# Kernel optimization log

Measured on AMD Instinct MI355X. Metric: run time of the kernel, lower is better.

The kernel has to match this reference:

```python
import jax, jax.numpy as jnp
import numpy as np
import math

B, T, D = 4, 4096, 256


def setup_inputs() -> dict:
    key = jax.random.key(0)
    ks = jax.random.split(key, 12)
    stdv = 1.0 / math.sqrt(D)
    u = lambda k, shape, s: jax.random.uniform(k, shape, jnp.float32, -s, s)
    return {
        "query": jax.random.normal(ks[0], (B, T, D), jnp.float32),
        "value": jax.random.normal(ks[1], (B, T, D), jnp.float32),
        # gate vectors, init uniform(-1/sqrt(D), 1/sqrt(D)) per reset_parameters
        "q_vec": u(ks[2], (D,), stdv),
        "k_vec": u(ks[3], (D,), stdv),
        "v_vec": u(ks[4], (D,), stdv),
        # nn.Linear params (torch default init: uniform(-1/sqrt(fan_in), ...))
        "Wq": u(ks[5], (D, D), stdv), "bq": u(ks[6], (D,), stdv),
        "Ws": u(ks[7], (D, D), stdv), "bs": u(ks[8], (D,), stdv),
        "Wt": u(ks[9], (D, D), stdv), "bt": u(ks[10], (D,), stdv),
    }


def reference(query, value, q_vec, k_vec, v_vec, Wq, bq, Ws, bs, Wt, bt):
    d = query.shape[-1]
    # q = Linear(query) * sigmoid(query_vector)
    q = (jnp.einsum('btd,ed->bte', query, Wq) + bq) * jax.nn.sigmoid(q_vec)
    # k = value * sigmoid(key_vector)
    k = value * jax.nn.sigmoid(k_vec)
    # v gate: infer=False branch -> GLU-style gate of sigmoid(value_vector)
    vv = jax.nn.sigmoid(v_vec)
    v_gate = jax.nn.sigmoid(Ws @ vv + bs) * jnp.tanh(Wt @ vv + bt)
    v = value * v_gate
    # scores [B, T, T]
    w = jnp.einsum('bqd,bkd->bqk', q, k) / jnp.sqrt(jnp.float32(d))
    # causal: multiply by tril mask then replace exact zeros with -inf
    # (faithful to the original's weight[weight==0]=-inf quirk)
    Tn = w.shape[-1]
    tril = jnp.tril(jnp.ones((Tn, Tn), w.dtype))
    w = w * tril
    w = jnp.where(w == 0.0, -jnp.inf, w)
    attn = jax.nn.softmax(w, axis=-1)
    return jnp.einsum('bqk,bkd->bqd', attn, v)
```

## Files before the change

### kernel.cpp

```cpp
#include <hip/hip_runtime.h>
#include <math.h>

#define D 256
#define T 4096
#define KT (17408/2)
#define VT (20480/2)
#define PSTR ((size_t)4*T*D)

typedef __attribute__((ext_vector_type(8))) short bf16x8;
typedef __attribute__((ext_vector_type(4))) float f32x4;
typedef __attribute__((ext_vector_type(8))) unsigned short u16x8;
typedef __attribute__((ext_vector_type(4))) unsigned int u32x4;

#define QSCALE 0.0901684850f

__device__ __forceinline__ unsigned short f2bf(float x){
  unsigned int u = __float_as_uint(x);
  unsigned int r = (u + 0x7FFFu + ((u >> 16) & 1u)) >> 16;
  return (unsigned short)r;
}
__device__ __forceinline__ float bf2f(unsigned short h){
  return __uint_as_float(((unsigned int)h) << 16);
}
__device__ __forceinline__ unsigned int cvtpk(float lo, float hi){
  unsigned int w;
  asm("v_cvt_pk_bf16_f32 %0, %1, %2" : "=v"(w) : "v"(lo), "v"(hi));
  return w;
}

__device__ __forceinline__ void gl_lds16(const void* g, void* l){
  __builtin_amdgcn_global_load_lds((const __attribute__((address_space(1))) unsigned int*)g,
                                   (__attribute__((address_space(3))) unsigned int*)l, 16, 0, 0);
}

__global__ __launch_bounds__(256) void prep_kernel(
    const float* __restrict__ q_vec, const float* __restrict__ k_vec,
    const float* __restrict__ v_vec, const float* __restrict__ Ws,
    const float* __restrict__ bs, const float* __restrict__ Wt,
    const float* __restrict__ bt, const float* __restrict__ Wq,
    float* __restrict__ gates, unsigned short* __restrict__ wq_g){
  int t = threadIdx.x;
  if(blockIdx.x == 0){
    __shared__ float vv[D];
    vv[t]         = 1.f/(1.f + __expf(-v_vec[t]));
    gates[t]      = 1.f/(1.f + __expf(-q_vec[t]));
    gates[D + t]  = 1.f/(1.f + __expf(-k_vec[t]));
    __syncthreads();
    const f32x4* wsr = (const f32x4*)(Ws + (size_t)t*D);
    const f32x4* wtr = (const f32x4*)(Wt + (size_t)t*D);
    const f32x4* vvv = (const f32x4*)vv;
    f32x4 a0 = {0,0,0,0}, a1 = {0,0,0,0}, c0 = {0,0,0,0}, c1 = {0,0,0,0};
    for(int i=0;i<64;i+=2){
      f32x4 v0 = vvv[i], v1 = vvv[i+1];
      a0 += wsr[i]*v0; a1 += wsr[i+1]*v1;
      c0 += wtr[i]*v0; c1 += wtr[i+1]*v1;
    }
    f32x4 as = a0 + a1, cs = c0 + c1;
    float s1 = bs[t] + as[0]+as[1]+as[2]+as[3];
    float s2 = bt[t] + cs[0]+cs[1]+cs[2]+cs[3];
    gates[2*D + t] = (1.f/(1.f + __expf(-s1))) * tanhf(s2);
  } else {
    int kc = blockIdx.x - 1;
    const float* src = Wq + (size_t)t*D + kc*32;
    unsigned short* dst = wq_g + (size_t)kc*10240 + t*40;
    #pragma unroll
    for(int u=0;u<4;u++){
      bf16x8 pk;
      #pragma unroll
      for(int x=0;x<8;x++) pk[x] = (short)f2bf(src[u*8+x]);
      *(bf16x8*)&dst[u*8] = pk;
    }
  }
}

__global__ __launch_bounds__(256) void mid_kernel(
    const float* __restrict__ query, const unsigned short* __restrict__ wq_g,
    const float* __restrict__ bq, const float* __restrict__ gates,
    unsigned short* __restrict__ q_g,
    const float* __restrict__ value,
    unsigned short* __restrict__ k_g, unsigned short* __restrict__ vt_g){
  __shared__ __align__(16) unsigned short smem[2][10240];
  int tid = threadIdx.x;
  if(blockIdx.x < 256){
    int w = tid >> 6; int l = tid & 63;
    int lr = l & 15, lc = l >> 4;
    int r0 = blockIdx.x * 64;
    f32x4 acc[16];
    #pragma unroll
    for(int n=0;n<16;n++) acc[n] = (f32x4){0.f,0.f,0.f,0.f};
    const float* qrow = query + (size_t)(r0 + w*16 + lr)*D;
    #pragma unroll
    for(int i=0;i<5;i++){ int c = i*256 + tid; gl_lds16(wq_g + c*8, (char*)smem[0] + c*16); }
    __syncthreads();
    int cur = 0;
    for(int kc=0; kc<8; kc++){
      if(kc < 7){
        #pragma unroll
        for(int i=0;i<5;i++){ int c = i*256 + tid;
          gl_lds16(wq_g + (size_t)(kc+1)*10240 + c*8, (char*)smem[cur^1] + c*16); }
      }
      bf16x8 af;
      {
        const float* s = qrow + kc*32 + lc*8;
        #pragma unroll
        for(int x=0;x<8;x++) af[x] = (short)f2bf(s[x]);
      }
      #pragma unroll
      for(int n=0;n<16;n++){
        bf16x8 bfrag = *(const bf16x8*)&smem[cur][(n*16 + lr)*40 + lc*8];
        acc[n] = __builtin_amdgcn_mfma_f32_16x16x32_bf16(af, bfrag, acc[n], 0, 0, 0);
      }
      __syncthreads();
      cur ^= 1;
    }
    #pragma unroll
    for(int n=0;n<16;n++){
      int col = n*16 + lr;
      float bb = bq[col], gg = gates[col] * QSCALE;
      #pragma unroll
      for(int r=0;r<4;r++){
        int row = r0 + w*16 + lc*4 + r;
        q_g[(size_t)row*D + col] = f2bf((acc[n][r] + bb) * gg);
      }
    }
  } else {
    int bid2 = blockIdx.x - 256;
    int b = bid2 >> 7, jt = bid2 & 127;
    const float* vbase = value + ((size_t)b*T + jt*32)*D;
    const float* gk = gates + D;
    const float* vg = gates + 2*D;
    unsigned short* kt = k_g  + (size_t)bid2 * KT;
    unsigned short* vt = vt_g + (size_t)bid2 * VT;
    #pragma unroll
    for(int i=0;i<4;i++){
      int g = i*256 + tid; int j = g >> 5, c = g & 31;
      const float* src = vbase + j*D + c*8;
      bf16x8 pk;
      #pragma unroll
      for(int x=0;x<8;x++) pk[x] = (short)f2bf(src[x] * gk[c*8+x]);
      *(bf16x8*)&kt[j*264 + c*8] = pk;
    }
    float* lds = (float*)smem;
    for(int c=0;c<4;c++){
      __syncthreads();
      {
        int row = tid >> 3, cg = tid & 7;
        const float* src = vbase + (size_t)row*D + c*64 + cg*8;
        f32x4 v0 = *(const f32x4*)src;
        f32x4 v1 = *(const f32x4*)(src + 4);
        *(f32x4*)&lds[row*68 + cg*8]     = v0;
        *(f32x4*)&lds[row*68 + cg*8 + 4] = v1;
      }
      __syncthreads();
      {
        int d0l = tid >> 2, u = tid & 3;
        int d0 = c*64 + d0l;
        float gd = vg[d0];
        bf16x8 pk;
        #pragma unroll
        for(int x=0;x<8;x++){
          int p = u*8 + x;
          int ksrc = ((p>>3)<<2) + (p&3) + (((p>>2)&1)<<4);
          pk[x] = (short)f2bf(lds[ksrc*68 + d0l] * gd);
        }
        *(bf16x8*)&vt[d0*40 + u*8] = pk;
      }
    }
  }
}

__global__ __launch_bounds__(256, 2) void flash_kernel(
    const unsigned short* __restrict__ q_g,
    const unsigned short* __restrict__ k_g,
    const unsigned short* __restrict__ vt_g,
    unsigned short* __restrict__ parts,
    float* __restrict__ ml, int logS){
  __shared__ __align__(16) unsigned short kbuf[2][KT];
  __shared__ __align__(16) unsigned short vbuf[2][VT];
  int tid = threadIdx.x; int w = tid >> 6, l = tid & 63;
  int lr = l & 15, lc = l >> 4;
  int S = 1 << logS;
  int bid = blockIdx.x;
  int x = bid & 7; int b = x >> 1; int p = x & 1;
  int item = bid >> 3;
  int half = S >> 1;
  int rblk = 31 - (item / half);
  int s = p*half + (item % half);
  int r0 = rblk * 128;
  int wrow0 = r0 + w*32;
  int nt = 4*rblk + 4;
  int jt0 = (s*nt) >> logS, jt1 = ((s+1)*nt) >> logS;
  int grA = wrow0 + lr;
  int grB = wrow0 + 16 + lr;
  int diagA = (wrow0 + 15) >> 5;
  int diagB = (wrow0 + 31) >> 5;

  bf16x8 qfA[8], qfB[8];
  {
    const unsigned short* qa = q_g + ((size_t)b*T + grA)*D + lc*8;
    const unsigned short* qb = q_g + ((size_t)b*T + grB)*D + lc*8;
    #pragma unroll
    for(int kc=0;kc<8;kc++){
      qfA[kc] = *(const bf16x8*)(qa + kc*32);
      qfB[kc] = *(const bf16x8*)(qb + kc*32);
    }
  }
  f32x4 oA[16], oB[16];
  #pragma unroll
  for(int n=0;n<16;n++){ oA[n] = (f32x4){0.f,0.f,0.f,0.f}; oB[n] = (f32x4){0.f,0.f,0.f,0.f}; }
  float mA = -INFINITY, lsA = 0.f, mB = -INFINITY, lsB = 0.f;

  const unsigned short* ktb = k_g  + (size_t)b*128*KT;
  const unsigned short* vtb = vt_g + (size_t)b*128*VT;

  if(jt1 > jt0){
    const unsigned short* ks = ktb + (size_t)jt0*KT;
    const unsigned short* vs = vtb + (size_t)jt0*VT;
    for(int c=w; c<37; c+=4){
      if(c < 17) gl_lds16(ks + c*512 + l*8, (char*)kbuf[jt0&1] + c*1024);
      else       gl_lds16(vs + (c-17)*512 + l*8, (char*)vbuf[jt0&1] + (c-17)*1024);
    }
  }

  for(int jt=jt0; jt<jt1; jt++){
    int cur = jt & 1;
    asm volatile("s_waitcnt vmcnt(0)" ::: "memory");
    __builtin_amdgcn_s_barrier();
    __builtin_amdgcn_sched_barrier(0);
    if(jt+1 < jt1){
      const unsigned short* ks = ktb + (size_t)(jt+1)*KT;
      const unsigned short* vs = vtb + (size_t)(jt+1)*VT;
      for(int c=w; c<37; c+=4){
        if(c < 17) gl_lds16(ks + c*512 + l*8, (char*)kbuf[cur^1] + c*1024);
        else       gl_lds16(vs + (c-17)*512 + l*8, (char*)vbuf[cur^1] + (c-17)*1024);
      }
    }
    int j0 = jt*32;
    bool actA = (j0 <= wrow0 + 15);
    bool actB = (j0 <= wrow0 + 31);
    if(actB){
      f32x4 sA0={0,0,0,0}, sA1={0,0,0,0}, sB0={0,0,0,0}, sB1={0,0,0,0};
      if(actA){
        #pragma unroll
        for(int kc=0;kc<8;kc++){
          bf16x8 k0 = *(const bf16x8*)&kbuf[cur][lr*264        + (kc*4 + lc)*8];
          bf16x8 k1 = *(const bf16x8*)&kbuf[cur][(16 + lr)*264 + (kc*4 + lc)*8];
          sA0 = __builtin_amdgcn_mfma_f32_16x16x32_bf16(k0, qfA[kc], sA0, 0,0,0);
          sA1 = __builtin_amdgcn_mfma_f32_16x16x32_bf16(k1, qfA[kc], sA1, 0,0,0);
          sB0 = __builtin_amdgcn_mfma_f32_16x16x32_bf16(k0, qfB[kc], sB0, 0,0,0);
          sB1 = __builtin_amdgcn_mfma_f32_16x16x32_bf16(k1, qfB[kc], sB1, 0,0,0);
        }
      } else {
        #pragma unroll
        for(int kc=0;kc<8;kc++){
          bf16x8 k0 = *(const bf16x8*)&kbuf[cur][lr*264        + (kc*4 + lc)*8];
          bf16x8 k1 = *(const bf16x8*)&kbuf[cur][(16 + lr)*264 + (kc*4 + lc)*8];
          sB0 = __builtin_amdgcn_mfma_f32_16x16x32_bf16(k0, qfB[kc], sB0, 0,0,0);
          sB1 = __builtin_amdgcn_mfma_f32_16x16x32_bf16(k1, qfB[kc], sB1, 0,0,0);
        }
      }
      bf16x8 paA, paB;
      if(actA){
        float sv0[4], sv1[4];
        if(jt == diagA){
          #pragma unroll
          for(int r=0;r<4;r++){
            float x0 = sA0[r]; int gj0 = j0 + lc*4 + r;
            float x1 = sA1[r]; int gj1 = gj0 + 16;
            sv0[r] = (gj0 > grA || x0 == 0.0f) ? -INFINITY : x0;
            sv1[r] = (gj1 > grA || x1 == 0.0f) ? -INFINITY : x1;
          }
        } else {
          #pragma unroll
          for(int r=0;r<4;r++){
            sv0[r] = (sA0[r] == 0.0f) ? -INFINITY : sA0[r];
            sv1[r] = (sA1[r] == 0.0f) ? -INFINITY : sA1[r];
          }
        }
        float pmax = fmaxf(fmaxf(fmaxf(sv0[0],sv0[1]),fmaxf(sv0[2],sv0[3])),
                           fmaxf(fmaxf(sv1[0],sv1[1]),fmaxf(sv1[2],sv1[3])));
        pmax = fmaxf(pmax, __shfl_xor(pmax, 16));
        pmax = fmaxf(pmax, __shfl_xor(pmax, 32));
        bool mv = (pmax > mA + 11.5f);
        float mn = mv ? pmax : mA;
        float alpha = mv ? exp2f(mA - mn) : 1.0f;
        float p0[4], p1[4];
        #pragma unroll
        for(int r=0;r<4;r++){
          p0[r] = exp2f(sv0[r] - mn);
          p1[r] = exp2f(sv1[r] - mn);
        }
        if(__builtin_amdgcn_ballot_w64(mv)){
          float a0 = __shfl(alpha, lc*4 + 0);
          float a1 = __shfl(alpha, lc*4 + 1);
          float a2 = __shfl(alpha, lc*4 + 2);
          float a3 = __shfl(alpha, lc*4 + 3);
          #pragma unroll
          for(int n=0;n<16;n++){
            oA[n][0] *= a0; oA[n][1] *= a1; oA[n][2] *= a2; oA[n][3] *= a3;
          }
        }
        float ps = ((p0[0]+p0[1])+(p0[2]+p0[3])) + ((p1[0]+p1[1])+(p1[2]+p1[3]));
        lsA = lsA*alpha + ps;
        mA = mn;
        union { unsigned int u[4]; bf16x8 h; } pu;
        pu.u[0] = cvtpk(p0[0], p0[1]); pu.u[1] = cvtpk(p0[2], p0[3]);
        pu.u[2] = cvtpk(p1[0], p1[1]); pu.u[3] = cvtpk(p1[2], p1[3]);
        paA = pu.h;
      }
      {
        float sv0[4], sv1[4];
        if(jt == diagB){
          #pragma unroll
          for(int r=0;r<4;r++){
            float x0 = sB0[r]; int gj0 = j0 + lc*4 + r;
            float x1 = sB1[r]; int gj1 = gj0 + 16;
            sv0[r] = (gj0 > grB || x0 == 0.0f) ? -INFINITY : x0;
            sv1[r] = (gj1 > grB || x1 == 0.0f) ? -INFINITY : x1;
          }
        } else {
          #pragma unroll
          for(int r=0;r<4;r++){
            sv0[r] = (sB0[r] == 0.0f) ? -INFINITY : sB0[r];
            sv1[r] = (sB1[r] == 0.0f) ? -INFINITY : sB1[r];
          }
        }
        float pmax = fmaxf(fmaxf(fmaxf(sv0[0],sv0[1]),fmaxf(sv0[2],sv0[3])),
                           fmaxf(fmaxf(sv1[0],sv1[1]),fmaxf(sv1[2],sv1[3])));
        pmax = fmaxf(pmax, __shfl_xor(pmax, 16));
        pmax = fmaxf(pmax, __shfl_xor(pmax, 32));
        bool mv = (pmax > mB + 11.5f);
        float mn = mv ? pmax : mB;
        float alpha = mv ? exp2f(mB - mn) : 1.0f;
        float p0[4], p1[4];
        #pragma unroll
        for(int r=0;r<4;r++){
          p0[r] = exp2f(sv0[r] - mn);
          p1[r] = exp2f(sv1[r] - mn);
        }
        if(__builtin_amdgcn_ballot_w64(mv)){
          float a0 = __shfl(alpha, lc*4 + 0);
          float a1 = __shfl(alpha, lc*4 + 1);
          float a2 = __shfl(alpha, lc*4 + 2);
          float a3 = __shfl(alpha, lc*4 + 3);
          #pragma unroll
          for(int n=0;n<16;n++){
            oB[n][0] *= a0; oB[n][1] *= a1; oB[n][2] *= a2; oB[n][3] *= a3;
          }
        }
        float ps = ((p0[0]+p0[1])+(p0[2]+p0[3])) + ((p1[0]+p1[1])+(p1[2]+p1[3]));
        lsB = lsB*alpha + ps;
        mB = mn;
        union { unsigned int u[4]; bf16x8 h; } pu;
        pu.u[0] = cvtpk(p0[0], p0[1]); pu.u[1] = cvtpk(p0[2], p0[3]);
        pu.u[2] = cvtpk(p1[0], p1[1]); pu.u[3] = cvtpk(p1[2], p1[3]);
        paB = pu.h;
      }
      if(actA){
        #pragma unroll
        for(int n=0;n<16;n++){
          bf16x8 vf = *(const bf16x8*)&vbuf[cur][(n*16 + lr)*40 + lc*8];
          oA[n] = __builtin_amdgcn_mfma_f32_16x16x32_bf16(paA, vf, oA[n], 0,0,0);
          oB[n] = __builtin_amdgcn_mfma_f32_16x16x32_bf16(paB, vf, oB[n], 0,0,0);
        }
      } else {
        #pragma unroll
        for(int n=0;n<16;n++){
          bf16x8 vf = *(const bf16x8*)&vbuf[cur][(n*16 + lr)*40 + lc*8];
          oB[n] = __builtin_amdgcn_mfma_f32_16x16x32_bf16(paB, vf, oB[n], 0,0,0);
        }
      }
    }
  }

  unsigned short* obase = parts + (size_t)s*PSTR + ((size_t)b*T + wrow0)*D;
  #pragma unroll
  for(int r=0;r<4;r++){
    int row = lc*4 + r;
    unsigned int wa[8], wb[8];
    #pragma unroll
    for(int k=0;k<8;k++){
      wa[k] = cvtpk(oA[2*k][r], oA[2*k+1][r]);
      wb[k] = cvtpk(oB[2*k][r], oB[2*k+1][r]);
    }
    *(u32x4*)&obase[(size_t)row*D + lr*16]          = (u32x4){wa[0],wa[1],wa[2],wa[3]};
    *(u32x4*)&obase[(size_t)row*D + lr*16 + 8]      = (u32x4){wa[4],wa[5],wa[6],wa[7]};
    *(u32x4*)&obase[(size_t)(row+16)*D + lr*16]     = (u32x4){wb[0],wb[1],wb[2],wb[3]};
    *(u32x4*)&obase[(size_t)(row+16)*D + lr*16 + 8] = (u32x4){wb[4],wb[5],wb[6],wb[7]};
  }
  lsA += __shfl_xor(lsA, 16); lsA += __shfl_xor(lsA, 32);
  lsB += __shfl_xor(lsB, 16); lsB += __shfl_xor(lsB, 32);
  if(l < 16){
    float* mlbA = ml + ((size_t)s*4*T + (size_t)b*T + wrow0 + lr)*2;
    mlbA[0] = mA; mlbA[1] = lsA;
    float* mlbB = ml + ((size_t)s*4*T + (size_t)b*T + wrow0 + 16 + lr)*2;
    mlbB[0] = mB; mlbB[1] = lsB;
  }
}

__global__ __launch_bounds__(256) void combine_kernel(
    const unsigned short* __restrict__ parts, const float* __restrict__ ml,
    float* __restrict__ out, int S){
  int t = blockIdx.x*256 + threadIdx.x;
  int row = t >> 4;
  int lr  = t & 15;
  float msv[8], lsv[8];
  float mm = -INFINITY;
  #pragma unroll
  for(int s=0;s<8;s++){
    if(s >= S) break;
    msv[s] = ml[((size_t)s*4*T + row)*2];
    lsv[s] = ml[((size_t)s*4*T + row)*2 + 1];
    mm = fmaxf(mm, msv[s]);
  }
  float denom = 0.f;
  float acc[16];
  #pragma unroll
  for(int n=0;n<16;n++) acc[n] = 0.f;
  #pragma unroll
  for(int s=0;s<8;s++){
    if(s >= S) break;
    float as = exp2f(msv[s] - mm);
    if(as != 0.0f){
      denom += as*lsv[s];
      const unsigned short* src = parts + (size_t)s*PSTR + (size_t)row*D + lr*16;
      u16x8 v0 = *(const u16x8*)src;
      u16x8 v1 = *(const u16x8*)(src + 8);
      #pragma unroll
      for(int n=0;n<8;n++){ acc[n] += as*bf2f(v0[n]); acc[8+n] += as*bf2f(v1[n]); }
    }
  }
  float inv = 1.0f/denom;
  float* orow = out + (size_t)row*D;
  #pragma unroll
  for(int n=0;n<16;n++) orow[n*16 + lr] = acc[n]*inv;
}

extern "C" void kernel_launch(void* const* d_in, const int* in_sizes, int n_in,
                              void* d_out, int out_size, void* d_ws, size_t ws_size,
                              hipStream_t stream){
  (void)in_sizes; (void)n_in; (void)out_size;
  const float* query = (const float*)d_in[0];
  const float* value = (const float*)d_in[1];
  const float* q_vec = (const float*)d_in[2];
  const float* k_vec = (const float*)d_in[3];
  const float* v_vec = (const float*)d_in[4];
  const float* Wq    = (const float*)d_in[5];
  const float* bq    = (const float*)d_in[6];
  const float* Ws    = (const float*)d_in[7];
  const float* bs    = (const float*)d_in[8];
  const float* Wt    = (const float*)d_in[9];
  const float* bt    = (const float*)d_in[10];
  char* ws = (char*)d_ws;
  unsigned short* q_g  = (unsigned short*)(ws);
  unsigned short* k_g  = (unsigned short*)(ws + 8388608);
  unsigned short* vt_g = (unsigned short*)(ws + 17301504);
  unsigned short* wq_g = (unsigned short*)(ws + 27787264);
  float* gates         = (float*)(ws + 27951104);
  unsigned short* parts= (unsigned short*)(ws + 27955200);
  float* out = (float*)d_out;

  size_t base = 27955200;
  size_t mlsz = (size_t)8*4*T*2*4;
  int logS;
  if(ws_size >= base + 8*PSTR*2 + mlsz)      logS = 3;
  else if(ws_size >= base + 4*PSTR*2 + mlsz) logS = 2;
  else                                       logS = 1;
  int S = 1 << logS;
  float* ml = (float*)(ws + base + (size_t)S*PSTR*2);

  hipLaunchKernelGGL(prep_kernel, dim3(9),   dim3(256), 0, stream,
                     q_vec, k_vec, v_vec, Ws, bs, Wt, bt, Wq, gates, wq_g);
  hipLaunchKernelGGL(mid_kernel,  dim3(768), dim3(256), 0, stream,
                     query, wq_g, bq, gates, q_g, value, k_g, vt_g);
  hipLaunchKernelGGL(flash_kernel, dim3(128*S), dim3(256), 0, stream,
                     q_g, k_g, vt_g, parts, ml, logS);
  hipLaunchKernelGGL(combine_kernel, dim3((4*T*16)/256), dim3(256), 0, stream,
                     parts, ml, out, S);
}
```

Baseline: 113.6 us.

## Fuse split-KV combine into flash kernel via last-block atomic counter

Removes the separate combine kernel. Each flash block bumps a per-(batch,row-block) atomic counter, and the last split to finish merges all partial outputs for that 128-row block and writes the final result. The work-to-block mapping also changes so the split index is the fastest-varying part of the block id, with row blocks interleaved by parity. This saves one launch and lets the combine overlap with other blocks, but it adds a memset, a fence plus atomic per block, and a serial tail in which a single block does the combine.

```diff
diff --git a/kernel.cpp b/kernel.cpp
--- a/kernel.cpp
+++ b/kernel.cpp
@@ -174,18 +174,20 @@
     const unsigned short* __restrict__ k_g,
     const unsigned short* __restrict__ vt_g,
     unsigned short* __restrict__ parts,
-    float* __restrict__ ml, int logS){
+    float* __restrict__ ml, unsigned int* __restrict__ cnt,
+    float* __restrict__ out, int logS){
   __shared__ __align__(16) unsigned short kbuf[2][KT];
   __shared__ __align__(16) unsigned short vbuf[2][VT];
+  __shared__ unsigned int lastflag;
   int tid = threadIdx.x; int w = tid >> 6, l = tid & 63;
   int lr = l & 15, lc = l >> 4;
   int S = 1 << logS;
   int bid = blockIdx.x;
-  int x = bid & 7; int b = x >> 1; int p = x & 1;
+  int x = bid & 7; int b = x >> 1; int par = x & 1;
   int item = bid >> 3;
-  int half = S >> 1;
-  int rblk = 31 - (item / half);
-  int s = p*half + (item % half);
+  int rl = item >> logS;
+  int rblk = (par ? 31 : 30) - 2*rl;
+  int s = item & (S - 1);
   int r0 = rblk * 128;
   int wrow0 = r0 + w*32;
   int nt = 4*rblk + 4;
@@ -396,44 +398,52 @@
     float* mlbB = ml + ((size_t)s*4*T + (size_t)b*T + wrow0 + 16 + lr)*2;
     mlbB[0] = mB; mlbB[1] = lsB;
   }
-}
-
-__global__ __launch_bounds__(256) void combine_kernel(
-    const unsigned short* __restrict__ parts, const float* __restrict__ ml,
-    float* __restrict__ out, int S){
-  int t = blockIdx.x*256 + threadIdx.x;
-  int row = t >> 4;
-  int lr  = t & 15;
-  float msv[8], lsv[8];
-  float mm = -INFINITY;
-  #pragma unroll
-  for(int s=0;s<8;s++){
-    if(s >= S) break;
-    msv[s] = ml[((size_t)s*4*T + row)*2];
-    lsv[s] = ml[((size_t)s*4*T + row)*2 + 1];
-    mm = fmaxf(mm, msv[s]);
-  }
-  float denom = 0.f;
-  float acc[16];
-  #pragma unroll
-  for(int n=0;n<16;n++) acc[n] = 0.f;
-  #pragma unroll
-  for(int s=0;s<8;s++){
-    if(s >= S) break;
-    float as = exp2f(msv[s] - mm);
-    if(as != 0.0f){
-      denom += as*lsv[s];
-      const unsigned short* src = parts + (size_t)s*PSTR + (size_t)row*D + lr*16;
-      u16x8 v0 = *(const u16x8*)src;
-      u16x8 v1 = *(const u16x8*)(src + 8);
-      #pragma unroll
-      for(int n=0;n<8;n++){ acc[n] += as*bf2f(v0[n]); acc[8+n] += as*bf2f(v1[n]); }
-    }
-  }
-  float inv = 1.0f/denom;
-  float* orow = out + (size_t)row*D;
-  #pragma unroll
-  for(int n=0;n<16;n++) orow[n*16 + lr] = acc[n]*inv;
+
+  __syncthreads();
+  if(tid == 0){
+    __threadfence();
+    unsigned int old = __hip_atomic_fetch_add(&cnt[b*32 + rblk], 1u,
+                         __ATOMIC_ACQ_REL, __HIP_MEMORY_SCOPE_AGENT);
+    lastflag = (old == (unsigned)(S - 1)) ? 1u : 0u;
+  }
+  __syncthreads();
+  if(!lastflag) return;
+
+  for(int it=0; it<8; it++){
+    int t2 = it*256 + tid;
+    int row = b*T + r0 + (t2 >> 4);
+    int lr2 = t2 & 15;
+    float msv[8], lsv[8];
+    float mm = -INFINITY;
+    #pragma unroll
+    for(int s2=0; s2<8; s2++){
+      if(s2 >= S) break;
+      msv[s2] = ml[((size_t)s2*4*T + row)*2];
+      lsv[s2] = ml[((size_t)s2*4*T + row)*2 + 1];
+      mm = fmaxf(mm, msv[s2]);
+    }
+    float denom = 0.f;
+    float acc[16];
+    #pragma unroll
+    for(int n=0;n<16;n++) acc[n] = 0.f;
+    #pragma unroll
+    for(int s2=0; s2<8; s2++){
+      if(s2 >= S) break;
+      float as = exp2f(msv[s2] - mm);
+      if(as != 0.0f){
+        denom += as*lsv[s2];
+        const unsigned short* src = parts + (size_t)s2*PSTR + (size_t)row*D + lr2*16;
+        u16x8 v0 = *(const u16x8*)src;
+        u16x8 v1 = *(const u16x8*)(src + 8);
+        #pragma unroll
+        for(int n=0;n<8;n++){ acc[n] += as*bf2f(v0[n]); acc[8+n] += as*bf2f(v1[n]); }
+      }
+    }
+    float inv = 1.0f/denom;
+    float* orow = out + (size_t)row*D;
+    #pragma unroll
+    for(int n=0;n<16;n++) orow[n*16 + lr2] = acc[n]*inv;
+  }
 }
 
 extern "C" void kernel_launch(void* const* d_in, const int* in_sizes, int n_in,
@@ -463,18 +473,18 @@
   size_t base = 27955200;
   size_t mlsz = (size_t)8*4*T*2*4;
   int logS;
-  if(ws_size >= base + 8*PSTR*2 + mlsz)      logS = 3;
-  else if(ws_size >= base + 4*PSTR*2 + mlsz) logS = 2;
-  else                                       logS = 1;
+  if(ws_size >= base + 8*PSTR*2 + mlsz + 512)      logS = 3;
+  else if(ws_size >= base + 4*PSTR*2 + mlsz + 512) logS = 2;
+  else                                             logS = 1;
   int S = 1 << logS;
   float* ml = (float*)(ws + base + (size_t)S*PSTR*2);
-
+  unsigned int* cnt = (unsigned int*)(ws + base + (size_t)S*PSTR*2 + mlsz);
+
+  hipMemsetAsync(cnt, 0, 512, stream);
   hipLaunchKernelGGL(prep_kernel, dim3(9),   dim3(256), 0, stream,
                      q_vec, k_vec, v_vec, Ws, bs, Wt, bt, Wq, gates, wq_g);
   hipLaunchKernelGGL(mid_kernel,  dim3(768), dim3(256), 0, stream,
                      query, wq_g, bq, gates, q_g, value, k_g, vt_g);
   hipLaunchKernelGGL(flash_kernel, dim3(128*S), dim3(256), 0, stream,
-                     q_g, k_g, vt_g, parts, ml, logS);
-  hipLaunchKernelGGL(combine_kernel, dim3((4*T*16)/256), dim3(256), 0, stream,
-                     parts, ml, out, S);
-}
+                     q_g, k_g, vt_g, parts, ml, cnt, out, logS);
+}
```

Result: slower. 225.7 us (+98.7%).

## Compute QK^T scores with FP8 MFMA using FP8 Q and swizzled FP8 K

Applied to the files above, without the earlier changes.

Q and K are now stored as FP8 instead of BF16. The score product uses the 16x16x32 fp8 MFMA, and the softmax scale is applied after the matmul instead of being folded into Q. K tiles drop their padded row stride and use an XOR swizzle for LDS bank-conflict avoidance, which halves K load traffic and LDS footprint per tile. This risks accuracy loss from FP8 quantization and may change which scores compare exactly equal to zero.

```diff
diff --git a/kernel.cpp b/kernel.cpp
--- a/kernel.cpp
+++ b/kernel.cpp
@@ -3,7 +3,7 @@
 
 #define D 256
 #define T 4096
-#define KT (17408/2)
+#define KTB 8192
 #define VT (20480/2)
 #define PSTR ((size_t)4*T*D)
 
@@ -25,6 +25,11 @@
 __device__ __forceinline__ unsigned int cvtpk(float lo, float hi){
   unsigned int w;
   asm("v_cvt_pk_bf16_f32 %0, %1, %2" : "=v"(w) : "v"(lo), "v"(hi));
+  return w;
+}
+__device__ __forceinline__ unsigned int cvtpk8(float lo, float hi){
+  unsigned int w;
+  asm("v_cvt_pk_fp8_f32 %0, %1, %2" : "=v"(w) : "v"(lo), "v"(hi));
   return w;
 }
 
@@ -76,9 +81,9 @@
 __global__ __launch_bounds__(256) void mid_kernel(
     const float* __restrict__ query, const unsigned short* __restrict__ wq_g,
     const float* __restrict__ bq, const float* __restrict__ gates,
-    unsigned short* __restrict__ q_g,
+    unsigned char* __restrict__ q8,
     const float* __restrict__ value,
-    unsigned short* __restrict__ k_g, unsigned short* __restrict__ vt_g){
+    unsigned char* __restrict__ k8, unsigned short* __restrict__ vt_g){
   __shared__ __align__(16) unsigned short smem[2][10240];
   int tid = threadIdx.x;
   if(blockIdx.x < 256){
@@ -116,12 +121,18 @@
     #pragma unroll
     for(int n=0;n<16;n++){
       int col = n*16 + lr;
-      float bb = bq[col], gg = gates[col] * QSCALE;
-      #pragma unroll
-      for(int r=0;r<4;r++){
-        int row = r0 + w*16 + lc*4 + r;
-        q_g[(size_t)row*D + col] = f2bf((acc[n][r] + bb) * gg);
-      }
+      float bb = bq[col], gg = gates[col];
+      float v0 = (acc[n][0] + bb) * gg;
+      float v1 = (acc[n][1] + bb) * gg;
+      float v2 = (acc[n][2] + bb) * gg;
+      float v3 = (acc[n][3] + bb) * gg;
+      unsigned int wlo = cvtpk8(v0, v1);
+      unsigned int whi = cvtpk8(v2, v3);
+      int row0 = r0 + w*16 + lc*4;
+      q8[(size_t)(row0+0)*D + col] = (unsigned char)(wlo);
+      q8[(size_t)(row0+1)*D + col] = (unsigned char)(wlo >> 8);
+      q8[(size_t)(row0+2)*D + col] = (unsigned char)(whi);
+      q8[(size_t)(row0+3)*D + col] = (unsigned char)(whi >> 8);
     }
   } else {
     int bid2 = blockIdx.x - 256;
@@ -129,16 +140,23 @@
     const float* vbase = value + ((size_t)b*T + jt*32)*D;
     const float* gk = gates + D;
     const float* vg = gates + 2*D;
-    unsigned short* kt = k_g  + (size_t)bid2 * KT;
+    unsigned char* kt = k8 + (size_t)bid2 * KTB;
     unsigned short* vt = vt_g + (size_t)bid2 * VT;
     #pragma unroll
     for(int i=0;i<4;i++){
       int g = i*256 + tid; int j = g >> 5, c = g & 31;
       const float* src = vbase + j*D + c*8;
-      bf16x8 pk;
+      float f[8];
       #pragma unroll
-      for(int x=0;x<8;x++) pk[x] = (short)f2bf(src[x] * gk[c*8+x]);
-      *(bf16x8*)&kt[j*264 + c*8] = pk;
+      for(int x=0;x<8;x++) f[x] = src[x] * gk[c*8+x];
+      unsigned int a0 = cvtpk8(f[0], f[1]);
+      unsigned int a1 = cvtpk8(f[2], f[3]);
+      unsigned int a2 = cvtpk8(f[4], f[5]);
+      unsigned int a3 = cvtpk8(f[6], f[7]);
+      unsigned long lo = (unsigned long)((a0 & 0xffffu) | (a1 << 16));
+      unsigned long hi = (unsigned long)((a2 & 0xffffu) | (a3 << 16));
+      unsigned int off = (unsigned)(c*8) ^ (unsigned)((j & 7) << 3);
+      *(unsigned long*)&kt[(size_t)j*256 + off] = lo | (hi << 32);
     }
     float* lds = (float*)smem;
     for(int c=0;c<4;c++){
@@ -170,12 +188,12 @@
 }
 
 __global__ __launch_bounds__(256, 2) void flash_kernel(
-    const unsigned short* __restrict__ q_g,
-    const unsigned short* __restrict__ k_g,
+    const unsigned char* __restrict__ q8,
+    const unsigned char* __restrict__ k8,
     const unsigned short* __restrict__ vt_g,
     unsigned short* __restrict__ parts,
     float* __restrict__ ml, int logS){
-  __shared__ __align__(16) unsigned short kbuf[2][KT];
+  __shared__ __align__(16) unsigned char kbuf8[2][KTB];
   __shared__ __align__(16) unsigned short vbuf[2][VT];
   int tid = threadIdx.x; int w = tid >> 6, l = tid & 63;
   int lr = l & 15, lc = l >> 4;
@@ -195,14 +213,14 @@
   int diagA = (wrow0 + 15) >> 5;
   int diagB = (wrow0 + 31) >> 5;
 
-  bf16x8 qfA[8], qfB[8];
+  long qfA[8], qfB[8];
   {
-    const unsigned short* qa = q_g + ((size_t)b*T + grA)*D + lc*8;
-    const unsigned short* qb = q_g + ((size_t)b*T + grB)*D + lc*8;
+    const unsigned char* qa = q8 + ((size_t)b*T + grA)*D + lc*8;
+    const unsigned char* qb = q8 + ((size_t)b*T + grB)*D + lc*8;
     #pragma unroll
     for(int kc=0;kc<8;kc++){
-      qfA[kc] = *(const bf16x8*)(qa + kc*32);
-      qfB[kc] = *(const bf16x8*)(qb + kc*32);
+      qfA[kc] = *(const long*)(qa + kc*32);
+      qfB[kc] = *(const long*)(qb + kc*32);
     }
   }
   f32x4 oA[16], oB[16];
@@ -210,15 +228,15 @@
   for(int n=0;n<16;n++){ oA[n] = (f32x4){0.f,0.f,0.f,0.f}; oB[n] = (f32x4){0.f,0.f,0.f,0.f}; }
   float mA = -INFINITY, lsA = 0.f, mB = -INFINITY, lsB = 0.f;
 
-  const unsigned short* ktb = k_g  + (size_t)b*128*KT;
+  const unsigned char*  ktb = k8   + (size_t)b*128*KTB;
   const unsigned short* vtb = vt_g + (size_t)b*128*VT;
 
   if(jt1 > jt0){
-    const unsigned short* ks = ktb + (size_t)jt0*KT;
+    const unsigned char*  ks = ktb + (size_t)jt0*KTB;
     const unsigned short* vs = vtb + (size_t)jt0*VT;
-    for(int c=w; c<37; c+=4){
-      if(c < 17) gl_lds16(ks + c*512 + l*8, (char*)kbuf[jt0&1] + c*1024);
-      else       gl_lds16(vs + (c-17)*512 + l*8, (char*)vbuf[jt0&1] + (c-17)*1024);
+    for(int c=w; c<28; c+=4){
+      if(c < 8) gl_lds16(ks + c*1024 + l*16, (char*)kbuf8[jt0&1] + c*1024);
+      else      gl_lds16(vs + (c-8)*512 + l*8, (char*)vbuf[jt0&1] + (c-8)*1024);
     }
   }
 
@@ -228,35 +246,39 @@
     __builtin_amdgcn_s_barrier();
     __builtin_amdgcn_sched_barrier(0);
     if(jt+1 < jt1){
-      const unsigned short* ks = ktb + (size_t)(jt+1)*KT;
+      const unsigned char*  ks = ktb + (size_t)(jt+1)*KTB;
       const unsigned short* vs = vtb + (size_t)(jt+1)*VT;
-      for(int c=w; c<37; c+=4){
-        if(c < 17) gl_lds16(ks + c*512 + l*8, (char*)kbuf[cur^1] + c*1024);
-        else       gl_lds16(vs + (c-17)*512 + l*8, (char*)vbuf[cur^1] + (c-17)*1024);
+      for(int c=w; c<28; c+=4){
+        if(c < 8) gl_lds16(ks + c*1024 + l*16, (char*)kbuf8[cur^1] + c*1024);
+        else      gl_lds16(vs + (c-8)*512 + l*8, (char*)vbuf[cur^1] + (c-8)*1024);
       }
     }
     int j0 = jt*32;
     bool actA = (j0 <= wrow0 + 15);
     bool actB = (j0 <= wrow0 + 31);
     if(actB){
+      const unsigned char* kb = kbuf8[cur];
+      unsigned soff = ((unsigned)(lr & 7)) << 3;
       f32x4 sA0={0,0,0,0}, sA1={0,0,0,0}, sB0={0,0,0,0}, sB1={0,0,0,0};
       if(actA){
         #pragma unroll
         for(int kc=0;kc<8;kc++){
-          bf16x8 k0 = *(const bf16x8*)&kbuf[cur][lr*264        + (kc*4 + lc)*8];
-          bf16x8 k1 = *(const bf16x8*)&kbuf[cur][(16 + lr)*264 + (kc*4 + lc)*8];
-          sA0 = __builtin_amdgcn_mfma_f32_16x16x32_bf16(k0, qfA[kc], sA0, 0,0,0);
-          sA1 = __builtin_amdgcn_mfma_f32_16x16x32_bf16(k1, qfA[kc], sA1, 0,0,0);
-          sB0 = __builtin_amdgcn_mfma_f32_16x16x32_bf16(k0, qfB[kc], sB0, 0,0,0);
-          sB1 = __builtin_amdgcn_mfma_f32_16x16x32_bf16(k1, qfB[kc], sB1, 0,0,0);
+          unsigned off = ((unsigned)((kc*4 + lc)*8)) ^ soff;
+          long k0 = *(const long*)&kb[(unsigned)lr*256 + off];
+          long k1 = *(const long*)&kb[(unsigned)(16 + lr)*256 + off];
+          sA0 = __builtin_amdgcn_mfma_f32_16x16x32_fp8_fp8(k0, qfA[kc], sA0, 0,0,0);
+          sA1 = __builtin_amdgcn_mfma_f32_16x16x32_fp8_fp8(k1, qfA[kc], sA1, 0,0,0);
+          sB0 = __builtin_amdgcn_mfma_f32_16x16x32_fp8_fp8(k0, qfB[kc], sB0, 0,0,0);
+          sB1 = __builtin_amdgcn_mfma_f32_16x16x32_fp8_fp8(k1, qfB[kc], sB1, 0,0,0);
         }
       } else {
         #pragma unroll
         for(int kc=0;kc<8;kc++){
-          bf16x8 k0 = *(const bf16x8*)&kbuf[cur][lr*264        + (kc*4 + lc)*8];
-          bf16x8 k1 = *(const bf16x8*)&kbuf[cur][(16 + lr)*264 + (kc*4 + lc)*8];
-          sB0 = __builtin_amdgcn_mfma_f32_16x16x32_bf16(k0, qfB[kc], sB0, 0,0,0);
-          sB1 = __builtin_amdgcn_mfma_f32_16x16x32_bf16(k1, qfB[kc], sB1, 0,0,0);
+          unsigned off = ((unsigned)((kc*4 + lc)*8)) ^ soff;
+          long k0 = *(const long*)&kb[(unsigned)lr*256 + off];
+          long k1 = *(const long*)&kb[(unsigned)(16 + lr)*256 + off];
+          sB0 = __builtin_amdgcn_mfma_f32_16x16x32_fp8_fp8(k0, qfB[kc], sB0, 0,0,0);
+          sB1 = __builtin_amdgcn_mfma_f32_16x16x32_fp8_fp8(k1, qfB[kc], sB1, 0,0,0);
         }
       }
       bf16x8 paA, paB;
@@ -265,16 +287,18 @@
         if(jt == diagA){
           #pragma unroll
           for(int r=0;r<4;r++){
-            float x0 = sA0[r]; int gj0 = j0 + lc*4 + r;
-            float x1 = sA1[r]; int gj1 = gj0 + 16;
+            float x0 = sA0[r]*QSCALE; int gj0 = j0 + lc*4 + r;
+            float x1 = sA1[r]*QSCALE; int gj1 = gj0 + 16;
             sv0[r] = (gj0 > grA || x0 == 0.0f) ? -INFINITY : x0;
             sv1[r] = (gj1 > grA || x1 == 0.0f) ? -INFINITY : x1;
           }
         } else {
           #pragma unroll
           for(int r=0;r<4;r++){
-            sv0[r] = (sA0[r] == 0.0f) ? -INFINITY : sA0[r];
-            sv1[r] = (sA1[r] == 0.0f) ? -INFINITY : sA1[r];
+            float x0 = sA0[r]*QSCALE;
+            float x1 = sA1[r]*QSCALE;
+            sv0[r] = (x0 == 0.0f) ? -INFINITY : x0;
+            sv1[r] = (x1 == 0.0f) ? -INFINITY : x1;
           }
         }
         float pmax = fmaxf(fmaxf(fmaxf(sv0[0],sv0[1]),fmaxf(sv0[2],sv0[3])),
@@ -313,16 +337,18 @@
         if(jt == diagB){
           #pragma unroll
           for(int r=0;r<4;r++){
-            float x0 = sB0[r]; int gj0 = j0 + lc*4 + r;
-            float x1 = sB1[r]; int gj1 = gj0 + 16;
+            float x0 = sB0[r]*QSCALE; int gj0 = j0 + lc*4 + r;
+            float x1 = sB1[r]*QSCALE; int gj1 = gj0 + 16;
             sv0[r] = (gj0 > grB || x0 == 0.0f) ? -INFINITY : x0;
             sv1[r] = (gj1 > grB || x1 == 0.0f) ? -INFINITY : x1;
           }
         } else {
           #pragma unroll
           for(int r=0;r<4;r++){
-            sv0[r] = (sB0[r] == 0.0f) ? -INFINITY : sB0[r];
-            sv1[r] = (sB1[r] == 0.0f) ? -INFINITY : sB1[r];
+            float x0 = sB0[r]*QSCALE;
+            float x1 = sB1[r]*QSCALE;
+            sv0[r] = (x0 == 0.0f) ? -INFINITY : x0;
+            sv1[r] = (x1 == 0.0f) ? -INFINITY : x1;
           }
         }
         float pmax = fmaxf(fmaxf(fmaxf(sv0[0],sv0[1]),fmaxf(sv0[2],sv0[3])),
@@ -452,8 +478,8 @@
   const float* Wt    = (const float*)d_in[9];
   const float* bt    = (const float*)d_in[10];
   char* ws = (char*)d_ws;
-  unsigned short* q_g  = (unsigned short*)(ws);
-  unsigned short* k_g  = (unsigned short*)(ws + 8388608);
+  unsigned char*  q8   = (unsigned char*)(ws);
+  unsigned char*  k8   = (unsigned char*)(ws + 8388608);
   unsigned short* vt_g = (unsigned short*)(ws + 17301504);
   unsigned short* wq_g = (unsigned short*)(ws + 27787264);
   float* gates         = (float*)(ws + 27951104);
@@ -472,9 +498,9 @@
   hipLaunchKernelGGL(prep_kernel, dim3(9),   dim3(256), 0, stream,
                      q_vec, k_vec, v_vec, Ws, bs, Wt, bt, Wq, gates, wq_g);
   hipLaunchKernelGGL(mid_kernel,  dim3(768), dim3(256), 0, stream,
-                     query, wq_g, bq, gates, q_g, value, k_g, vt_g);
+                     query, wq_g, bq, gates, q8, value, k8, vt_g);
   hipLaunchKernelGGL(flash_kernel, dim3(128*S), dim3(256), 0, stream,
-                     q_g, k_g, vt_g, parts, ml, logS);
+                     q8, k8, vt_g, parts, ml, logS);
   hipLaunchKernelGGL(combine_kernel, dim3((4*T*16)/256), dim3(256), 0, stream,
                      parts, ml, out, S);
 }
```

Measured after the change: 111.9 us. No clear change (-1.5%).
